# Kernel optimization log

Measured on AMD Instinct MI355X. Metric: run time of the kernel, lower is better.

## Reference

```python
import jax, jax.numpy as jnp
import numpy as np

N_QUBITS = 4
N_QLAYERS = 2
CNOT_PAIRS = [(0, 1), (1, 2), (2, 3), (3, 0)]  # fixed ring entangler; RZ angle uses W[target]


def _apply_1q(psi, U, q):
    # psi: [B,2,2,2,2]; U: [2,2] (shared angle) or [B,2,2] (per-sample angle)
    psi2 = jnp.moveaxis(psi, q + 1, -1)
    if U.ndim == 3:
        out = jnp.einsum('bij,b...j->b...i', U, psi2)
    else:
        out = jnp.einsum('ij,b...j->b...i', U, psi2)
    return jnp.moveaxis(out, -1, q + 1)


def _rx(theta):
    # RX(t) = [[cos t/2, -i sin t/2], [-i sin t/2, cos t/2]]; works for scalar or [B]
    c = jnp.cos(theta / 2).astype(jnp.complex64)
    s = (-1j) * jnp.sin(theta / 2).astype(jnp.complex64)
    return jnp.stack([jnp.stack([c, s], -1), jnp.stack([s, c], -1)], -2)


def _rz(theta):
    # RZ(t) = diag(e^{-it/2}, e^{it/2})
    tc = theta.astype(jnp.complex64)
    p = jnp.exp(-0.5j * tc)
    q = jnp.exp(0.5j * tc)
    z = jnp.zeros_like(p)
    return jnp.stack([jnp.stack([p, z], -1), jnp.stack([z, q], -1)], -2)


def _cnot(psi, c, t):
    ca, ta = c + 1, t + 1
    s0 = jax.lax.slice_in_dim(psi, 0, 1, axis=ca)
    s1 = jnp.flip(jax.lax.slice_in_dim(psi, 1, 2, axis=ca), axis=ta)
    return jnp.concatenate([s0, s1], axis=ca)


def _circuit(y, w):
    # y: [B,4] embedding angles (AngleEmbedding default = RX); w: [n_qlayers,4]
    B = y.shape[0]
    psi = jnp.zeros((B, 2, 2, 2, 2), jnp.complex64).at[:, 0, 0, 0, 0].set(1.0)
    for q in range(N_QUBITS):
        psi = _apply_1q(psi, _rx(y[:, q]), q)
    for l in range(N_QLAYERS):
        W = w[l]
        for q in range(N_QUBITS):
            psi = _apply_1q(psi, _rx(W[q]), q)
            psi = _apply_1q(psi, _rz(W[q]), q)
            psi = _apply_1q(psi, _rx(W[q]), q)
        for c, t in CNOT_PAIRS:
            psi = _cnot(psi, c, t)
            psi = _apply_1q(psi, _rz(W[t]), t)
            psi = _cnot(psi, c, t)
    probs = psi.real ** 2 + psi.imag ** 2  # [B,2,2,2,2]
    sgn = jnp.array([1.0, -1.0], jnp.float32)
    z = []
    for q in range(N_QUBITS):
        shp = [1] * 5
        shp[q + 1] = 2
        z.append(jnp.sum(probs * sgn.reshape(shp), axis=(1, 2, 3, 4)))
    return jnp.stack(z, -1)  # [B,4] PauliZ expectations


def setup_inputs() -> dict:
    key = jax.random.key(0)
    ks = jax.random.split(key, 6)
    B, T, F, H, Q = 8192, 128, 64, 128, 4
    return {
        'x': jax.random.normal(ks[0], (B, T, F), jnp.float32),
        'W_in': jax.random.normal(ks[1], (Q, H + F), jnp.float32) * 0.1,
        'b_in': jax.random.normal(ks[2], (Q,), jnp.float32) * 0.1,
        'q_weights': jax.random.normal(ks[3], (N_QLAYERS, Q), jnp.float32),
        'W_out': jax.random.normal(ks[4], (H, Q), jnp.float32) * 0.1,
        'b_out': jax.random.normal(ks[5], (H,), jnp.float32) * 0.1,
    }


def reference(x, W_in, b_in, q_weights, W_out, b_out):
    B = x.shape[0]
    H = W_out.shape[0]
    h0 = jnp.zeros((B, H), x.dtype)
    xs = jnp.swapaxes(x, 0, 1)  # [T,B,F]

    def step(h, x_t):
        v = jnp.concatenate([h, x_t], axis=1)  # cat (h_t, x_t) as in source
        y = v @ W_in.T + b_in
        z = _circuit(y, q_weights)
        h_new = jax.nn.sigmoid(z @ W_out.T + b_out)
        return h_new, None

    h_T, _ = jax.lax.scan(step, h0, xs)
    return h_T
```

## Files before the change

kernel.cpp:

```cpp
#include <hip/hip_runtime.h>


struct Cpx { float x, y; };
__device__ __forceinline__ Cpx cmul(Cpx a, Cpx b){ return {a.x*b.x - a.y*b.y, a.x*b.y + a.y*b.x}; }
__device__ __forceinline__ Cpx cadd(Cpx a, Cpx b){ return {a.x + b.x, a.y + b.y}; }

__global__ void qrnn_precompute(const float* __restrict__ qw, float* __restrict__ C)
{
    __shared__ Cpx U[16][16];
    __shared__ Cpx M[4][16][16];
    const int tid = threadIdx.x;

    if (tid == 0) {
        for (int i = 0; i < 16; ++i)
            for (int j = 0; j < 16; ++j)
                U[i][j] = Cpx{(i == j) ? 1.f : 0.f, 0.f};

        for (int l = 0; l < 2; ++l) {
            for (int q = 0; q < 4; ++q) {
                float w  = qw[l*4 + q];
                float ch = cosf(0.5f*w), sh = sinf(0.5f*w);
                Cpx RX[2][2] = {{{ch,0.f},{0.f,-sh}},{{0.f,-sh},{ch,0.f}}};
                Cpx RZ[2][2] = {{{ch,-sh},{0.f,0.f}},{{0.f,0.f},{ch,sh}}};
                Cpx T[2][2], A[2][2];
                for (int i = 0; i < 2; ++i)
                    for (int j = 0; j < 2; ++j) {
                        Cpx s{0.f,0.f};
                        for (int k = 0; k < 2; ++k) s = cadd(s, cmul(RZ[i][k], RX[k][j]));
                        T[i][j] = s;
                    }
                for (int i = 0; i < 2; ++i)
                    for (int j = 0; j < 2; ++j) {
                        Cpx s{0.f,0.f};
                        for (int k = 0; k < 2; ++k) s = cadd(s, cmul(RX[i][k], T[k][j]));
                        A[i][j] = s;
                    }
                int bit = 1 << (3 - q);
                for (int r = 0; r < 16; ++r) {
                    if (r & bit) continue;
                    int r1 = r | bit;
                    for (int j = 0; j < 16; ++j) {
                        Cpx a0 = U[r][j], a1 = U[r1][j];
                        U[r][j]  = cadd(cmul(A[0][0], a0), cmul(A[0][1], a1));
                        U[r1][j] = cadd(cmul(A[1][0], a0), cmul(A[1][1], a1));
                    }
                }
            }
            for (int e = 0; e < 4; ++e) {
                int c = e, t = (e + 1) & 3;
                float th = qw[l*4 + t];
                float ch = cosf(0.5f*th), sh = sinf(0.5f*th);
                Cpx pe{ch,-sh}, pd{ch,sh};
                int bc = 1 << (3 - c), bt = 1 << (3 - t);
                for (int r = 0; r < 16; ++r) {
                    bool eq = (((r & bc) != 0) == ((r & bt) != 0));
                    Cpx ph = eq ? pe : pd;
                    for (int j = 0; j < 16; ++j) U[r][j] = cmul(ph, U[r][j]);
                }
            }
        }
    }
    __syncthreads();

    for (int e = tid; e < 4*16*16; e += blockDim.x) {
        int k = e >> 8, i = (e >> 4) & 15, j = e & 15;
        int kb = 1 << (3 - k);
        Cpx s{0.f,0.f};
        for (int m = 0; m < 16; ++m) {
            float sg = (m & kb) ? -1.f : 1.f;
            Cpx um = U[m][i]; um.y = -um.y;
            Cpx t  = cmul(um, U[m][j]);
            s.x += sg * t.x; s.y += sg * t.y;
        }
        M[k][i][j] = s;
    }
    __syncthreads();

    for (int e = tid; e < 4*81; e += blockDim.x) {
        int k = e / 81, a = e % 81;
        int d[4], aa = a;
        for (int q = 0; q < 4; ++q) { d[q] = aa % 3; aa /= 3; }
        int ym = 0, ny = 0;
        for (int q = 0; q < 4; ++q) if (d[q] == 2) { ym |= 1 << (3 - q); ++ny; }
        Cpx tr{0.f,0.f};
        for (int i = 0; i < 16; ++i) {
            int j = i ^ ym;
            Cpx p{1.f,0.f};
            for (int q = 0; q < 4; ++q) {
                int bi = (i >> (3 - q)) & 1;
                if (d[q] == 1) { if (bi) { p.x = -p.x; p.y = -p.y; } }
                else if (d[q] == 2) {
                    Cpx f = bi ? Cpx{0.f,1.f} : Cpx{0.f,-1.f};
                    p = cmul(p, f);
                }
            }
            tr = cadd(tr, cmul(p, M[k][j][i]));
        }
        float val = tr.x * 0.0625f;
        if (ny & 1) val = -val;
        C[k*81 + a] = val;
    }
}


__global__ __launch_bounds__(256) void qrnn_main(
    const float* __restrict__ x,
    const float* __restrict__ W_in,
    const float* __restrict__ b_in,
    const float* __restrict__ W_out,
    const float* __restrict__ b_out,
    const float* __restrict__ C,
    float* __restrict__ out,
    int B)
{
    const int lane = threadIdx.x & 63;
    const int wv   = threadIdx.x >> 6;
    const int slot = lane >> 4;
    const int sl   = lane & 15;
    const int b    = blockIdx.x * 16 + wv * 4 + slot;
    const int bc   = (b < B) ? b : (B - 1);

    float wa[4][8], wx[4][4];
    #pragma unroll
    for (int q = 0; q < 4; ++q) {
        #pragma unroll
        for (int j = 0; j < 8; ++j) wa[q][j] = W_in[q*192 + sl + 16*j];
        #pragma unroll
        for (int u = 0; u < 4; ++u) wx[q][u] = W_in[q*192 + 128 + 4*sl + u];
    }
    const int kown = sl & 3;
    const int grp  = sl >> 2;
    const float bi_own = b_in[kown];

    const int cbase = kown*81 + 27*((grp < 3) ? grp : 2);
    float cc[27];
    #pragma unroll
    for (int m = 0; m < 27; ++m) cc[m] = C[cbase + m];
    const bool zact = (grp < 3);

    float wo[8][4], bo[8];
    #pragma unroll
    for (int j = 0; j < 8; ++j) {
        #pragma unroll
        for (int k = 0; k < 4; ++k) wo[j][k] = W_out[(sl + 16*j)*4 + k];
        bo[j] = b_out[sl + 16*j];
    }

    float h[8];
    #pragma unroll
    for (int j = 0; j < 8; ++j) h[j] = 0.f;

    const float* __restrict__ xb = x + (size_t)bc * (128*64) + 4*sl;
    float4 xcur = *(const float4*)(xb);
    float4 xnxt = *(const float4*)(xb + 64);

    const int gbase = lane & ~3;

    for (int t = 0; t < 128; ++t) {
        const int tp = (t + 2 < 128) ? (t + 2) : 127;
        const float4 xpre = *(const float4*)(xb + tp*64);

        float p0, p1, p2, p3;
        {
            p0 = wx[0][0]*xcur.x; p1 = wx[1][0]*xcur.x; p2 = wx[2][0]*xcur.x; p3 = wx[3][0]*xcur.x;
            p0 = fmaf(wx[0][1], xcur.y, p0); p1 = fmaf(wx[1][1], xcur.y, p1);
            p2 = fmaf(wx[2][1], xcur.y, p2); p3 = fmaf(wx[3][1], xcur.y, p3);
            p0 = fmaf(wx[0][2], xcur.z, p0); p1 = fmaf(wx[1][2], xcur.z, p1);
            p2 = fmaf(wx[2][2], xcur.z, p2); p3 = fmaf(wx[3][2], xcur.z, p3);
            p0 = fmaf(wx[0][3], xcur.w, p0); p1 = fmaf(wx[1][3], xcur.w, p1);
            p2 = fmaf(wx[2][3], xcur.w, p2); p3 = fmaf(wx[3][3], xcur.w, p3);
            #pragma unroll
            for (int j = 0; j < 8; ++j) {
                p0 = fmaf(wa[0][j], h[j], p0);
                p1 = fmaf(wa[1][j], h[j], p1);
                p2 = fmaf(wa[2][j], h[j], p2);
                p3 = fmaf(wa[3][j], h[j], p3);
            }
        }

        {
            const bool o1 = (sl & 1) != 0;
            const bool o2 = (sl & 2) != 0;
            float sendA = o1 ? p0 : p1;
            float a  = (o1 ? p1 : p0) + __shfl_xor(sendA, 1, 64);
            float sendB = o1 ? p2 : p3;
            float bq = (o1 ? p3 : p2) + __shfl_xor(sendB, 1, 64);
            float send2 = o2 ? a : bq;
            float s  = (o2 ? bq : a) + __shfl_xor(send2, 2, 64);
            s += __shfl_xor(s, 4, 64);
            s += __shfl_xor(s, 8, 64);
            p0 = s + bi_own;
        }
        const float y0 = __shfl(p0, gbase | 0, 64);
        const float y1 = __shfl(p0, gbase | 1, 64);
        const float y2 = __shfl(p0, gbase | 2, 64);
        const float y3 = __shfl(p0, gbase | 3, 64);

        float s0, c0, s1, c1, s2, c2, s3, c3;
        __sincosf(y0, &s0, &c0);
        __sincosf(y1, &s1, &c1);
        __sincosf(y2, &s2, &c2);
        __sincosf(y3, &s3, &c3);

        float zp;
        {
            float t0, t1, t2, i0, i1, i2;
            t0 = fmaf(s0, cc[ 2], fmaf(c0, cc[ 1], cc[ 0]));
            t1 = fmaf(s0, cc[ 5], fmaf(c0, cc[ 4], cc[ 3]));
            t2 = fmaf(s0, cc[ 8], fmaf(c0, cc[ 7], cc[ 6]));
            i0 = fmaf(s1, t2, fmaf(c1, t1, t0));
            t0 = fmaf(s0, cc[11], fmaf(c0, cc[10], cc[ 9]));
            t1 = fmaf(s0, cc[14], fmaf(c0, cc[13], cc[12]));
            t2 = fmaf(s0, cc[17], fmaf(c0, cc[16], cc[15]));
            i1 = fmaf(s1, t2, fmaf(c1, t1, t0));
            t0 = fmaf(s0, cc[20], fmaf(c0, cc[19], cc[18]));
            t1 = fmaf(s0, cc[23], fmaf(c0, cc[22], cc[21]));
            t2 = fmaf(s0, cc[26], fmaf(c0, cc[25], cc[24]));
            i2 = fmaf(s1, t2, fmaf(c1, t1, t0));
            const float mid = fmaf(s2, i2, fmaf(c2, i1, i0));
            const float g3v = (grp == 0) ? 1.f : ((grp == 1) ? c3 : s3);
            zp = zact ? g3v * mid : 0.f;
        }

        zp += __shfl_xor(zp, 4, 64);
        zp += __shfl_xor(zp, 8, 64);
        const float z0 = __shfl(zp, gbase | 0, 64);
        const float z1 = __shfl(zp, gbase | 1, 64);
        const float z2 = __shfl(zp, gbase | 2, 64);
        const float z3 = __shfl(zp, gbase | 3, 64);

        #pragma unroll
        for (int j = 0; j < 8; ++j) {
            float u = fmaf(wo[j][0], z0, fmaf(wo[j][1], z1,
                      fmaf(wo[j][2], z2, fmaf(wo[j][3], z3, bo[j]))));
            h[j] = 1.f / (1.f + __expf(-u));
        }

        xcur = xnxt; xnxt = xpre;
    }

    if (b < B) {
        float* ob = out + (size_t)b * 128 + sl;
        #pragma unroll
        for (int j = 0; j < 8; ++j) ob[16*j] = h[j];
    }
}

extern "C" void kernel_launch(void* const* d_in, const int* in_sizes, int n_in,
                              void* d_out, int out_size, void* d_ws, size_t ws_size,
                              hipStream_t stream)
{
    const float* x     = (const float*)d_in[0];
    const float* W_in  = (const float*)d_in[1];
    const float* b_in  = (const float*)d_in[2];
    const float* qw    = (const float*)d_in[3];
    const float* W_out = (const float*)d_in[4];
    const float* b_out = (const float*)d_in[5];
    float* out = (float*)d_out;
    float* C   = (float*)d_ws;

    const int B = in_sizes[0] / (128*64);

    qrnn_precompute<<<1, 128, 0, stream>>>(qw, C);
    const int blocks = (B + 15) / 16;
    qrnn_main<<<blocks, 256, 0, stream>>>(x, W_in, b_in, W_out, b_out, C, out, B);
}
```

Before: 624.2 us.

## Use 32 lanes per sample, DPP/swizzle reductions, parallel precompute

Each batch sample now gets 32 lanes instead of 16, so each lane holds half the hidden units and input features, and the 81-term observable polynomial is split across 9 lane groups with selector coefficients. Cross-lane shuffles are replaced by DPP and ds_swizzle intrinsics to cut the latency of the per-step reductions and broadcasts. The precompute kernel builds the unitary column-parallel across 16 threads instead of serially in one thread, and launch bounds now request occupancy 4. The trade-off is twice as many lanes per sample, which means more waves in total, and the swizzle patterns must line up with the new 32-lane grouping.

```diff
diff --git a/kernel.cpp b/kernel.cpp
--- a/kernel.cpp
+++ b/kernel.cpp
@@ -4,6 +4,16 @@
 struct Cpx { float x, y; };
 __device__ __forceinline__ Cpx cmul(Cpx a, Cpx b){ return {a.x*b.x - a.y*b.y, a.x*b.y + a.y*b.x}; }
 __device__ __forceinline__ Cpx cadd(Cpx a, Cpx b){ return {a.x + b.x, a.y + b.y}; }
+
+template<int CTRL>
+__device__ __forceinline__ float fdpp(float v) {
+    return __int_as_float(__builtin_amdgcn_update_dpp(
+        0, __float_as_int(v), CTRL, 0xF, 0xF, true));
+}
+template<int PAT>
+__device__ __forceinline__ float fswz(float v) {
+    return __int_as_float(__builtin_amdgcn_ds_swizzle(__float_as_int(v), PAT));
+}
 
 __global__ void qrnn_precompute(const float* __restrict__ qw, float* __restrict__ C)
 {
@@ -11,63 +21,72 @@
     __shared__ Cpx M[4][16][16];
     const int tid = threadIdx.x;
 
-    if (tid == 0) {
-        for (int i = 0; i < 16; ++i)
-            for (int j = 0; j < 16; ++j)
-                U[i][j] = Cpx{(i == j) ? 1.f : 0.f, 0.f};
+    if (tid < 16) {
+        Cpx col[16];
+        #pragma unroll
+        for (int i = 0; i < 16; ++i) col[i] = Cpx{(i == tid) ? 1.f : 0.f, 0.f};
 
         for (int l = 0; l < 2; ++l) {
-            for (int q = 0; q < 4; ++q) {
-                float w  = qw[l*4 + q];
-                float ch = cosf(0.5f*w), sh = sinf(0.5f*w);
-                Cpx RX[2][2] = {{{ch,0.f},{0.f,-sh}},{{0.f,-sh},{ch,0.f}}};
-                Cpx RZ[2][2] = {{{ch,-sh},{0.f,0.f}},{{0.f,0.f},{ch,sh}}};
-                Cpx T[2][2], A[2][2];
-                for (int i = 0; i < 2; ++i)
-                    for (int j = 0; j < 2; ++j) {
-                        Cpx s{0.f,0.f};
-                        for (int k = 0; k < 2; ++k) s = cadd(s, cmul(RZ[i][k], RX[k][j]));
-                        T[i][j] = s;
-                    }
-                for (int i = 0; i < 2; ++i)
-                    for (int j = 0; j < 2; ++j) {
-                        Cpx s{0.f,0.f};
-                        for (int k = 0; k < 2; ++k) s = cadd(s, cmul(RX[i][k], T[k][j]));
-                        A[i][j] = s;
-                    }
-                int bit = 1 << (3 - q);
+            #define APPLY_Q(qq, BIT)                                             \
+            {                                                                    \
+                const float w  = qw[l*4 + (qq)];                                 \
+                const float ch = cosf(0.5f*w), sh = sinf(0.5f*w);                \
+                const Cpx RX[2][2] = {{{ch,0.f},{0.f,-sh}},{{0.f,-sh},{ch,0.f}}};\
+                const Cpx RZ[2][2] = {{{ch,-sh},{0.f,0.f}},{{0.f,0.f},{ch,sh}}};\
+                Cpx T[2][2], A[2][2];                                            \
+                for (int i = 0; i < 2; ++i)                                      \
+                    for (int j = 0; j < 2; ++j) {                                \
+                        Cpx s{0.f,0.f};                                          \
+                        for (int k = 0; k < 2; ++k)                              \
+                            s = cadd(s, cmul(RZ[i][k], RX[k][j]));               \
+                        T[i][j] = s;                                             \
+                    }                                                            \
+                for (int i = 0; i < 2; ++i)                                      \
+                    for (int j = 0; j < 2; ++j) {                                \
+                        Cpx s{0.f,0.f};                                          \
+                        for (int k = 0; k < 2; ++k)                              \
+                            s = cadd(s, cmul(RX[i][k], T[k][j]));                \
+                        A[i][j] = s;                                             \
+                    }                                                            \
+                _Pragma("unroll")                                                \
+                for (int r = 0; r < 16; ++r) {                                   \
+                    if (r & (BIT)) continue;                                     \
+                    const int r1 = r | (BIT);                                    \
+                    Cpx a0 = col[r], a1 = col[r1];                               \
+                    col[r]  = cadd(cmul(A[0][0], a0), cmul(A[0][1], a1));        \
+                    col[r1] = cadd(cmul(A[1][0], a0), cmul(A[1][1], a1));        \
+                }                                                                \
+            }
+            APPLY_Q(0, 8)
+            APPLY_Q(1, 4)
+            APPLY_Q(2, 2)
+            APPLY_Q(3, 1)
+            #undef APPLY_Q
+
+            for (int e = 0; e < 4; ++e) {
+                const int c = e, t = (e + 1) & 3;
+                const float th = qw[l*4 + t];
+                const float ch = cosf(0.5f*th), sh = sinf(0.5f*th);
+                const Cpx pe{ch,-sh}, pd{ch,sh};
+                const int bc = 1 << (3 - c), bt = 1 << (3 - t);
+                #pragma unroll
                 for (int r = 0; r < 16; ++r) {
-                    if (r & bit) continue;
-                    int r1 = r | bit;
-                    for (int j = 0; j < 16; ++j) {
-                        Cpx a0 = U[r][j], a1 = U[r1][j];
-                        U[r][j]  = cadd(cmul(A[0][0], a0), cmul(A[0][1], a1));
-                        U[r1][j] = cadd(cmul(A[1][0], a0), cmul(A[1][1], a1));
-                    }
+                    const bool eq = (((r & bc) != 0) == ((r & bt) != 0));
+                    col[r] = cmul(eq ? pe : pd, col[r]);
                 }
             }
-            for (int e = 0; e < 4; ++e) {
-                int c = e, t = (e + 1) & 3;
-                float th = qw[l*4 + t];
-                float ch = cosf(0.5f*th), sh = sinf(0.5f*th);
-                Cpx pe{ch,-sh}, pd{ch,sh};
-                int bc = 1 << (3 - c), bt = 1 << (3 - t);
-                for (int r = 0; r < 16; ++r) {
-                    bool eq = (((r & bc) != 0) == ((r & bt) != 0));
-                    Cpx ph = eq ? pe : pd;
-                    for (int j = 0; j < 16; ++j) U[r][j] = cmul(ph, U[r][j]);
-                }
-            }
-        }
+        }
+        #pragma unroll
+        for (int i = 0; i < 16; ++i) U[i][tid] = col[i];
     }
     __syncthreads();
 
     for (int e = tid; e < 4*16*16; e += blockDim.x) {
-        int k = e >> 8, i = (e >> 4) & 15, j = e & 15;
-        int kb = 1 << (3 - k);
+        const int k = e >> 8, i = (e >> 4) & 15, j = e & 15;
+        const int kb = 1 << (3 - k);
         Cpx s{0.f,0.f};
         for (int m = 0; m < 16; ++m) {
-            float sg = (m & kb) ? -1.f : 1.f;
+            const float sg = (m & kb) ? -1.f : 1.f;
             Cpx um = U[m][i]; um.y = -um.y;
             Cpx t  = cmul(um, U[m][j]);
             s.x += sg * t.x; s.y += sg * t.y;
@@ -77,17 +96,17 @@
     __syncthreads();
 
     for (int e = tid; e < 4*81; e += blockDim.x) {
-        int k = e / 81, a = e % 81;
+        const int k = e / 81, a = e % 81;
         int d[4], aa = a;
         for (int q = 0; q < 4; ++q) { d[q] = aa % 3; aa /= 3; }
         int ym = 0, ny = 0;
         for (int q = 0; q < 4; ++q) if (d[q] == 2) { ym |= 1 << (3 - q); ++ny; }
         Cpx tr{0.f,0.f};
         for (int i = 0; i < 16; ++i) {
-            int j = i ^ ym;
+            const int j = i ^ ym;
             Cpx p{1.f,0.f};
             for (int q = 0; q < 4; ++q) {
-                int bi = (i >> (3 - q)) & 1;
+                const int bi = (i >> (3 - q)) & 1;
                 if (d[q] == 1) { if (bi) { p.x = -p.x; p.y = -p.y; } }
                 else if (d[q] == 2) {
                     Cpx f = bi ? Cpx{0.f,1.f} : Cpx{0.f,-1.f};
@@ -103,7 +122,7 @@
 }
 
 
-__global__ __launch_bounds__(256) void qrnn_main(
+__global__ __launch_bounds__(256, 4) void qrnn_main(
     const float* __restrict__ x,
     const float* __restrict__ W_in,
     const float* __restrict__ b_in,
@@ -115,86 +134,87 @@
 {
     const int lane = threadIdx.x & 63;
     const int wv   = threadIdx.x >> 6;
-    const int slot = lane >> 4;
-    const int sl   = lane & 15;
-    const int b    = blockIdx.x * 16 + wv * 4 + slot;
+    const int slot = lane >> 5;
+    const int sl   = lane & 31;
+    const int b    = blockIdx.x * 8 + wv * 2 + slot;
     const int bc   = (b < B) ? b : (B - 1);
 
-    float wa[4][8], wx[4][4];
+    float wa[4][4], wx[4][2];
     #pragma unroll
     for (int q = 0; q < 4; ++q) {
         #pragma unroll
-        for (int j = 0; j < 8; ++j) wa[q][j] = W_in[q*192 + sl + 16*j];
-        #pragma unroll
-        for (int u = 0; u < 4; ++u) wx[q][u] = W_in[q*192 + 128 + 4*sl + u];
+        for (int j = 0; j < 4; ++j) wa[q][j] = W_in[q*192 + sl + 32*j];
+        wx[q][0] = W_in[q*192 + 128 + 2*sl];
+        wx[q][1] = W_in[q*192 + 128 + 2*sl + 1];
     }
     const int kown = sl & 3;
     const int grp  = sl >> 2;
     const float bi_own = b_in[kown];
 
-    const int cbase = kown*81 + 27*((grp < 3) ? grp : 2);
-    float cc[27];
-    #pragma unroll
-    for (int m = 0; m < 27; ++m) cc[m] = C[cbase + m];
-    const bool zact = (grp < 3);
-
-    float wo[8][4], bo[8];
-    #pragma unroll
-    for (int j = 0; j < 8; ++j) {
-        #pragma unroll
-        for (int k = 0; k < 4; ++k) wo[j][k] = W_out[(sl + 16*j)*4 + k];
-        bo[j] = b_out[sl + 16*j];
-    }
-
-    float h[8];
-    #pragma unroll
-    for (int j = 0; j < 8; ++j) h[j] = 0.f;
-
-    const float* __restrict__ xb = x + (size_t)bc * (128*64) + 4*sl;
-    float4 xcur = *(const float4*)(xb);
-    float4 xnxt = *(const float4*)(xb + 64);
-
-    const int gbase = lane & ~3;
+    const int d3 = grp / 3, d2 = grp % 3;
+    float cc0[9], cc1[9];
+    #pragma unroll
+    for (int m = 0; m < 9; ++m) {
+        cc0[m] = C[kown*81 + 27*d3 + 9*d2 + m];
+        cc1[m] = (grp == 0) ? C[kown*81 + 72 + m] : 0.f;
+    }
+    const float o2i = (d2 == 0) ? 1.f : 0.f, o2c = (d2 == 1) ? 1.f : 0.f,
+                o2s = (d2 == 2) ? 1.f : 0.f;
+    const float o3i = (d3 == 0) ? 1.f : 0.f, o3c = (d3 == 1) ? 1.f : 0.f,
+                o3s = (d3 == 2) ? 1.f : 0.f;
+
+    float wo[4][4], bo[4];
+    #pragma unroll
+    for (int j = 0; j < 4; ++j) {
+        #pragma unroll
+        for (int k = 0; k < 4; ++k) wo[j][k] = W_out[(sl + 32*j)*4 + k];
+        bo[j] = b_out[sl + 32*j];
+    }
+
+    float h[4];
+    #pragma unroll
+    for (int j = 0; j < 4; ++j) h[j] = 0.f;
+
+    const float* __restrict__ xb = x + (size_t)bc * (128*64) + 2*sl;
+    float2 xcur = *(const float2*)(xb);
+    float2 xnxt = *(const float2*)(xb + 64);
 
     for (int t = 0; t < 128; ++t) {
         const int tp = (t + 2 < 128) ? (t + 2) : 127;
-        const float4 xpre = *(const float4*)(xb + tp*64);
+        const float2 xpre = *(const float2*)(xb + tp*64);
 
         float p0, p1, p2, p3;
-        {
-            p0 = wx[0][0]*xcur.x; p1 = wx[1][0]*xcur.x; p2 = wx[2][0]*xcur.x; p3 = wx[3][0]*xcur.x;
-            p0 = fmaf(wx[0][1], xcur.y, p0); p1 = fmaf(wx[1][1], xcur.y, p1);
-            p2 = fmaf(wx[2][1], xcur.y, p2); p3 = fmaf(wx[3][1], xcur.y, p3);
-            p0 = fmaf(wx[0][2], xcur.z, p0); p1 = fmaf(wx[1][2], xcur.z, p1);
-            p2 = fmaf(wx[2][2], xcur.z, p2); p3 = fmaf(wx[3][2], xcur.z, p3);
-            p0 = fmaf(wx[0][3], xcur.w, p0); p1 = fmaf(wx[1][3], xcur.w, p1);
-            p2 = fmaf(wx[2][3], xcur.w, p2); p3 = fmaf(wx[3][3], xcur.w, p3);
-            #pragma unroll
-            for (int j = 0; j < 8; ++j) {
-                p0 = fmaf(wa[0][j], h[j], p0);
-                p1 = fmaf(wa[1][j], h[j], p1);
-                p2 = fmaf(wa[2][j], h[j], p2);
-                p3 = fmaf(wa[3][j], h[j], p3);
-            }
-        }
-
+        p0 = wx[0][0]*xcur.x; p1 = wx[1][0]*xcur.x;
+        p2 = wx[2][0]*xcur.x; p3 = wx[3][0]*xcur.x;
+        p0 = fmaf(wx[0][1], xcur.y, p0); p1 = fmaf(wx[1][1], xcur.y, p1);
+        p2 = fmaf(wx[2][1], xcur.y, p2); p3 = fmaf(wx[3][1], xcur.y, p3);
+        #pragma unroll
+        for (int j = 0; j < 4; ++j) {
+            p0 = fmaf(wa[0][j], h[j], p0);
+            p1 = fmaf(wa[1][j], h[j], p1);
+            p2 = fmaf(wa[2][j], h[j], p2);
+            p3 = fmaf(wa[3][j], h[j], p3);
+        }
+
+        float yown;
         {
             const bool o1 = (sl & 1) != 0;
             const bool o2 = (sl & 2) != 0;
             float sendA = o1 ? p0 : p1;
-            float a  = (o1 ? p1 : p0) + __shfl_xor(sendA, 1, 64);
+            float a  = (o1 ? p1 : p0) + fdpp<0xB1>(sendA);
             float sendB = o1 ? p2 : p3;
-            float bq = (o1 ? p3 : p2) + __shfl_xor(sendB, 1, 64);
+            float bq = (o1 ? p3 : p2) + fdpp<0xB1>(sendB);
             float send2 = o2 ? a : bq;
-            float s  = (o2 ? bq : a) + __shfl_xor(send2, 2, 64);
-            s += __shfl_xor(s, 4, 64);
-            s += __shfl_xor(s, 8, 64);
-            p0 = s + bi_own;
-        }
-        const float y0 = __shfl(p0, gbase | 0, 64);
-        const float y1 = __shfl(p0, gbase | 1, 64);
-        const float y2 = __shfl(p0, gbase | 2, 64);
-        const float y3 = __shfl(p0, gbase | 3, 64);
+            float s  = (o2 ? bq : a) + fdpp<0x4E>(send2);
+            s += fswz<0x101F>(s);
+            s += fswz<0x201F>(s);
+            s += fswz<0x401F>(s);
+            yown = s + bi_own;
+        }
+        const float y0 = fdpp<0x00>(yown);
+        const float y1 = fdpp<0x55>(yown);
+        const float y2 = fdpp<0xAA>(yown);
+        const float y3 = fdpp<0xFF>(yown);
 
         float s0, c0, s1, c1, s2, c2, s3, c3;
         __sincosf(y0, &s0, &c0);
@@ -202,35 +222,33 @@
         __sincosf(y2, &s2, &c2);
         __sincosf(y3, &s3, &c3);
 
-        float zp;
+        const float f2  = fmaf(o2c, c2, fmaf(o2s, s2, o2i));
+        const float f3  = fmaf(o3c, c3, fmaf(o3s, s3, o3i));
+        const float f23 = f2 * f3;
+        const float f8  = s2 * s3;
+        float i0, i1;
         {
-            float t0, t1, t2, i0, i1, i2;
-            t0 = fmaf(s0, cc[ 2], fmaf(c0, cc[ 1], cc[ 0]));
-            t1 = fmaf(s0, cc[ 5], fmaf(c0, cc[ 4], cc[ 3]));
-            t2 = fmaf(s0, cc[ 8], fmaf(c0, cc[ 7], cc[ 6]));
+            float t0 = fmaf(s0, cc0[2], fmaf(c0, cc0[1], cc0[0]));
+            float t1 = fmaf(s0, cc0[5], fmaf(c0, cc0[4], cc0[3]));
+            float t2 = fmaf(s0, cc0[8], fmaf(c0, cc0[7], cc0[6]));
             i0 = fmaf(s1, t2, fmaf(c1, t1, t0));
-            t0 = fmaf(s0, cc[11], fmaf(c0, cc[10], cc[ 9]));
-            t1 = fmaf(s0, cc[14], fmaf(c0, cc[13], cc[12]));
-            t2 = fmaf(s0, cc[17], fmaf(c0, cc[16], cc[15]));
+            t0 = fmaf(s0, cc1[2], fmaf(c0, cc1[1], cc1[0]));
+            t1 = fmaf(s0, cc1[5], fmaf(c0, cc1[4], cc1[3]));
+            t2 = fmaf(s0, cc1[8], fmaf(c0, cc1[7], cc1[6]));
             i1 = fmaf(s1, t2, fmaf(c1, t1, t0));
-            t0 = fmaf(s0, cc[20], fmaf(c0, cc[19], cc[18]));
-            t1 = fmaf(s0, cc[23], fmaf(c0, cc[22], cc[21]));
-            t2 = fmaf(s0, cc[26], fmaf(c0, cc[25], cc[24]));
-            i2 = fmaf(s1, t2, fmaf(c1, t1, t0));
-            const float mid = fmaf(s2, i2, fmaf(c2, i1, i0));
-            const float g3v = (grp == 0) ? 1.f : ((grp == 1) ? c3 : s3);
-            zp = zact ? g3v * mid : 0.f;
-        }
-
-        zp += __shfl_xor(zp, 4, 64);
-        zp += __shfl_xor(zp, 8, 64);
-        const float z0 = __shfl(zp, gbase | 0, 64);
-        const float z1 = __shfl(zp, gbase | 1, 64);
-        const float z2 = __shfl(zp, gbase | 2, 64);
-        const float z3 = __shfl(zp, gbase | 3, 64);
-
-        #pragma unroll
-        for (int j = 0; j < 8; ++j) {
+        }
+        float zp = fmaf(f23, i0, f8 * i1);
+
+        zp += fswz<0x101F>(zp);
+        zp += fswz<0x201F>(zp);
+        zp += fswz<0x401F>(zp);
+        const float z0 = fdpp<0x00>(zp);
+        const float z1 = fdpp<0x55>(zp);
+        const float z2 = fdpp<0xAA>(zp);
+        const float z3 = fdpp<0xFF>(zp);
+
+        #pragma unroll
+        for (int j = 0; j < 4; ++j) {
             float u = fmaf(wo[j][0], z0, fmaf(wo[j][1], z1,
                       fmaf(wo[j][2], z2, fmaf(wo[j][3], z3, bo[j]))));
             h[j] = 1.f / (1.f + __expf(-u));
@@ -242,7 +260,7 @@
     if (b < B) {
         float* ob = out + (size_t)b * 128 + sl;
         #pragma unroll
-        for (int j = 0; j < 8; ++j) ob[16*j] = h[j];
+        for (int j = 0; j < 4; ++j) ob[32*j] = h[j];
     }
 }
 
@@ -261,7 +279,7 @@
 
     const int B = in_sizes[0] / (128*64);
 
-    qrnn_precompute<<<1, 128, 0, stream>>>(qw, C);
-    const int blocks = (B + 15) / 16;
+    qrnn_precompute<<<1, 64, 0, stream>>>(qw, C);
+    const int blocks = (B + 7) / 8;
     qrnn_main<<<blocks, 256, 0, stream>>>(x, W_in, b_in, W_out, b_out, C, out, B);
 }
```

After: 506.1 us. 18.9% less time.
